# Kernel tuning notes

Measured on AMD Instinct MI355X. Metric: run time of the kernel, lower is better.

Reference implementation:

```python
import jax, jax.numpy as jnp
import numpy as np

B, G, L, S = 4096, 16000, 64, 20000  # batch spots, genes, labels, total spots
LOG_2PI = float(np.log(2.0 * np.pi))


def _log_nb_positive_altparam(x, r, o):
    # NB with total_count r > 0 and logits o (stereoscope parametrization)
    return (jax.lax.lgamma(x + r) - jax.lax.lgamma(r) - jax.lax.lgamma(x + 1.0)
            + x * jax.nn.log_sigmoid(o) + r * jax.nn.log_sigmoid(-o))


def setup_inputs() -> dict:
    key = jax.random.key(0)
    ks = jax.random.split(key, 8)
    x = jax.random.randint(ks[0], (B, G), 0, 100, dtype=jnp.int32)
    y = jax.random.randint(ks[1], (B, 1), 0, L, dtype=jnp.int32)
    ind_x = jax.random.randint(ks[2], (B, 1), 0, S, dtype=jnp.int32)
    W = jax.random.normal(ks[3], (G, L), dtype=jnp.float32)          # fixed dictionary
    px_o = 0.5 * jax.random.normal(ks[4], (G,), dtype=jnp.float32)   # fixed log-odds
    eta = jax.random.normal(ks[5], (G,), dtype=jnp.float32)
    V = jax.random.normal(ks[6], (L + 1, S), dtype=jnp.float32)
    beta = 0.1 * jax.random.normal(ks[7], (G,), dtype=jnp.float32)
    return {"x": x, "y": y, "ind_x": ind_x, "W": W, "px_o": px_o,
            "eta": eta, "V": V, "beta": beta}


def reference(x, y, ind_x, W, px_o, eta, V, beta):
    x_f = x.astype(jnp.float32)                      # [B, G]
    beta_sp = jax.nn.softplus(beta)                  # [G]
    w_sp = jax.nn.softplus(W)                        # [G, L]
    eps_sp = jax.nn.softplus(eta)                    # [G]
    # r_hat = [beta*W | eps]  -> [G, L+1]
    r_hat = jnp.concatenate([beta_sp[:, None] * w_sp, eps_sp[:, None]], axis=1)
    # column-gather from V (embedding lookup over spots), then softplus
    v_ind = jax.nn.softplus(V[:, ind_x[:, 0]])       # [L+1, B]
    # thin matmul, inner dim L+1; px_rate: [B, G]
    px_rate = jnp.einsum("gl,lb->bg", r_hat, v_ind)
    # NB reconstruction loss per spot
    reconst_loss = -jnp.sum(_log_nb_positive_altparam(x_f, px_rate, px_o[None, :]), axis=-1)  # [B]
    # -sum log N(eta; 0, 1)
    neg_log_likelihood_prior = jnp.sum(0.5 * LOG_2PI + 0.5 * eta * eta)
    return (reconst_loss, jnp.float32(0.0), neg_log_likelihood_prior)
```

## Files before the change

kernel.cpp:

```cpp
#include <hip/hip_runtime.h>
#include <hip/hip_bf16.h>
#include <math.h>

#define Gn 16000
#define Bn 4096
#define Ln 64
#define Sn 20000
#define NGT 250

typedef __attribute__((ext_vector_type(8))) short bf16x8;
typedef __attribute__((ext_vector_type(4))) float f32x4;


__device__ __forceinline__ float softplus_precise(float z) {
    return fmaxf(z, 0.0f) + log1pf(__expf(-fabsf(z)));
}

__device__ __forceinline__ float lgamma_pos8(float z) {
    float p = z * (z + 1.f) * (z + 2.f) * (z + 3.f)
                * (z + 4.f) * (z + 5.f) * (z + 6.f) * (z + 7.f);
    float w = z + 8.f;
    return (w - 0.5f) * __logf(w) - w + 0.9189385332046727f
           + __fdividef(1.0f, 12.0f * w) - __logf(p);
}

__device__ __forceinline__ unsigned short f2bf(float f) {
    union { float f; unsigned int u; } v; v.f = f;
    unsigned int r = v.u + 0x7fff + ((v.u >> 16) & 1);
    return (unsigned short)(r >> 16);
}


__global__ void prep_genes(const float* __restrict__ W,
                           const float* __restrict__ px_o,
                           const float* __restrict__ eta,
                           const float* __restrict__ beta,
                           unsigned short* __restrict__ rhB,
                           float* __restrict__ lsp1,
                           float* __restrict__ lsn,
                           float* __restrict__ eps,
                           float* __restrict__ out) {
    int idx = blockIdx.x * 256 + threadIdx.x;
    int g = idx >> 6;
    float bsp = softplus_precise(beta[g]);
    rhB[idx] = f2bf(bsp * softplus_precise(W[idx]));
    float s = 0.f;
    if (idx < Gn) {
        eps[idx] = softplus_precise(eta[idx]);
        float o = px_o[idx];
        lsp1[idx] = -softplus_precise(-o) - 1.0f;
        lsn[idx]  = -softplus_precise(o);
        float e = eta[idx];
        s = 0.9189385332046727f + 0.5f * e * e;
    }
    #pragma unroll
    for (int off = 32; off; off >>= 1) s += __shfl_xor(s, off, 64);
    __shared__ float red[4];
    if ((threadIdx.x & 63) == 0) red[threadIdx.x >> 6] = s;
    __syncthreads();
    if (threadIdx.x == 0) {
        float t = red[0] + red[1] + red[2] + red[3];
        if (t != 0.f) atomicAdd(&out[Bn + 1], t);
    }
}

__global__ void prep_spots(const float* __restrict__ V,
                           const int* __restrict__ ind_x,
                           unsigned short* __restrict__ vBg,
                           float* __restrict__ v64) {
    int idx = blockIdx.x * 256 + threadIdx.x;
    int b = idx >> 6, l = idx & 63;
    int s = ind_x[b];
    vBg[idx] = f2bf(softplus_precise(V[l * Sn + s]));
    if (idx < Bn) {
        int s2 = ind_x[idx];
        v64[idx] = softplus_precise(V[Ln * Sn + s2]);
    }
}


__global__ __launch_bounds__(256) void main_kernel(
    const int*            __restrict__ x,
    const unsigned short* __restrict__ rhB,
    const unsigned short* __restrict__ vBg,
    const float*          __restrict__ v64,
    const float*          __restrict__ lsp1g,
    const float*          __restrict__ lsng,
    const float*          __restrict__ epsg,
    float*                __restrict__ partial) {
    __shared__ __align__(16) unsigned short sA[64][72];
    __shared__ __align__(16) unsigned short sB[64][72];
    __shared__ float sv64[64];
    __shared__ float sLsp1[64], sLsn[64], sEps[64];
    __shared__ float lfact[100];
    __shared__ float pred[64];

    const int tid = threadIdx.x;
    const int b0 = blockIdx.x * 64;
    const int g0 = blockIdx.y * 64;

    {
        int row = tid >> 3;
        int c   = (tid & 7) * 8;
        *(uint4*)&sA[row][c]      = *(const uint4*)&vBg[(b0 + row) * 64 + c];
        *(uint4*)&sA[row + 32][c] = *(const uint4*)&vBg[(b0 + row + 32) * 64 + c];
        *(uint4*)&sB[row][c]      = *(const uint4*)&rhB[(g0 + row) * 64 + c];
        *(uint4*)&sB[row + 32][c] = *(const uint4*)&rhB[(g0 + row + 32) * 64 + c];
    }
    if (tid < 64) {
        sv64[tid]  = v64[b0 + tid];
        sLsp1[tid] = lsp1g[g0 + tid];
        sLsn[tid]  = lsng[g0 + tid];
        sEps[tid]  = epsg[g0 + tid];
    }
    if (tid < 100) lfact[tid] = lgamma_pos8((float)tid + 1.0f);

    const int wave = tid >> 6, lane = tid & 63;
    const int quad = lane >> 4, ln = lane & 15;
    const int mrow  = wave * 16 + ln;
    const int brow0 = b0 + wave * 16 + quad * 4;

    int xv[4][4];
    #pragma unroll
    for (int nb = 0; nb < 4; nb++) {
        int g = g0 + nb * 16 + ln;
        #pragma unroll
        for (int r = 0; r < 4; r++)
            xv[nb][r] = x[(size_t)(brow0 + r) * Gn + g];
    }

    f32x4 acc[4];
    #pragma unroll
    for (int nb = 0; nb < 4; nb++) acc[nb] = (f32x4){0.f, 0.f, 0.f, 0.f};

    __syncthreads();

    #pragma unroll
    for (int kb = 0; kb < 2; kb++) {
        bf16x8 af = *(const bf16x8*)&sA[mrow][kb * 32 + quad * 8];
        #pragma unroll
        for (int nb = 0; nb < 4; nb++) {
            bf16x8 bfr = *(const bf16x8*)&sB[nb * 16 + ln][kb * 32 + quad * 8];
            acc[nb] = __builtin_amdgcn_mfma_f32_16x16x32_bf16(af, bfr, acc[nb], 0, 0, 0);
        }
    }

    float vvr[4];
    #pragma unroll
    for (int r = 0; r < 4; r++) vvr[r] = sv64[wave * 16 + quad * 4 + r];

    float rowpart[4] = {0.f, 0.f, 0.f, 0.f};
    #pragma unroll
    for (int nb = 0; nb < 4; nb++) {
        const float lsp1v = sLsp1[nb * 16 + ln];
        const float lsnv  = sLsn[nb * 16 + ln];
        const float ev    = sEps[nb * 16 + ln];
        #pragma unroll
        for (int r = 0; r < 4; r++) {
            const float rr = fmaf(ev, vvr[r], acc[nb][r]);
            const int   xi = xv[nb][r];
            const float xf = (float)xi;
            const float s  = rr + xf;
            float t = fmaf(s - 0.5f, __logf(s), -lfact[xi]);
            t = fmaf(-(rr - 0.5f), __logf(rr), t);
            t = fmaf(xf, lsp1v, t);
            t = fmaf(rr, lsnv, t);
            rowpart[r] += t;
        }
    }

    #pragma unroll
    for (int r = 0; r < 4; r++) {
        float v = rowpart[r];
        v += __shfl_xor(v, 1, 64);
        v += __shfl_xor(v, 2, 64);
        v += __shfl_xor(v, 4, 64);
        v += __shfl_xor(v, 8, 64);
        if (ln == 0) pred[wave * 16 + quad * 4 + r] = v;
    }
    __syncthreads();
    if (tid < 64) partial[(size_t)blockIdx.y * Bn + b0 + tid] = pred[tid];
}

__global__ __launch_bounds__(256) void reduce_kernel(const float* __restrict__ partial,
                                                     float* __restrict__ out) {
    int b = blockIdx.x * 256 + threadIdx.x;
    float s0 = 0.f, s1 = 0.f, s2 = 0.f, s3 = 0.f, s4 = 0.f;
    for (int i = 0; i < NGT; i += 5) {
        s0 += partial[(size_t)(i + 0) * Bn + b];
        s1 += partial[(size_t)(i + 1) * Bn + b];
        s2 += partial[(size_t)(i + 2) * Bn + b];
        s3 += partial[(size_t)(i + 3) * Bn + b];
        s4 += partial[(size_t)(i + 4) * Bn + b];
    }
    out[b] = -(s0 + s1 + s2 + s3 + s4);
}


extern "C" void kernel_launch(void* const* d_in, const int* in_sizes, int n_in,
                              void* d_out, int out_size, void* d_ws, size_t ws_size,
                              hipStream_t stream) {
    const int*   x     = (const int*)d_in[0];
    const int*   ind_x = (const int*)d_in[2];
    const float* W     = (const float*)d_in[3];
    const float* px_o  = (const float*)d_in[4];
    const float* eta   = (const float*)d_in[5];
    const float* V     = (const float*)d_in[6];
    const float* beta  = (const float*)d_in[7];
    float* out = (float*)d_out;

    char* wsb = (char*)d_ws;
    unsigned short* rhB  = (unsigned short*)(wsb);
    unsigned short* vBg  = (unsigned short*)(wsb + 2048000);
    float*          v64  = (float*)(wsb + 2572288);
    float*          lsp1 = (float*)(wsb + 2588672);
    float*          lsn  = (float*)(wsb + 2652672);
    float*          eps  = (float*)(wsb + 2716672);
    float*          part = (float*)(wsb + 2780672);

    hipMemsetAsync(d_out, 0, (Bn + 2) * sizeof(float), stream);

    prep_genes<<<(Gn * 64) / 256, 256, 0, stream>>>(W, px_o, eta, beta, rhB, lsp1, lsn, eps, out);
    prep_spots<<<(Bn * 64) / 256, 256, 0, stream>>>(V, ind_x, vBg, v64);

    dim3 grid(Bn / 64, Gn / 64);
    main_kernel<<<grid, 256, 0, stream>>>(x, rhB, vBg, v64, lsp1, lsn, eps, part);

    reduce_kernel<<<Bn / 256, 256, 0, stream>>>(part, out);
}
```

Before: 413.0 us.

## Fuse prep kernels, drop memset and atomic, reorder main grid gene-major

Merges the gene and spot preprocessing kernels into one launch that branches on block index. The memset and the atomic prior accumulation are replaced by per-block partial sums that the reduce kernel combines; the reduce kernel also writes the zero output directly. The main kernel's grid is swapped so adjacent blocks cover adjacent gene tiles of the same spot rows, which changes the DRAM and cache access order for the large x matrix. The goal is lower launch overhead and better locality, at the cost of a slightly larger reduce kernel.

```diff
diff --git a/kernel.cpp b/kernel.cpp
--- a/kernel.cpp
+++ b/kernel.cpp
@@ -7,6 +7,8 @@
 #define Ln 64
 #define Sn 20000
 #define NGT 250
+#define GENE_BLOCKS 4000
+#define SPOT_BLOCKS 1024
 
 typedef __attribute__((ext_vector_type(8))) short bf16x8;
 typedef __attribute__((ext_vector_type(4))) float f32x4;
@@ -31,50 +33,52 @@
 }
 
 
-__global__ void prep_genes(const float* __restrict__ W,
+__global__ void prep_fused(const float* __restrict__ W,
                            const float* __restrict__ px_o,
                            const float* __restrict__ eta,
                            const float* __restrict__ beta,
+                           const float* __restrict__ V,
+                           const int*   __restrict__ ind_x,
                            unsigned short* __restrict__ rhB,
                            float* __restrict__ lsp1,
                            float* __restrict__ lsn,
                            float* __restrict__ eps,
-                           float* __restrict__ out) {
-    int idx = blockIdx.x * 256 + threadIdx.x;
-    int g = idx >> 6;
-    float bsp = softplus_precise(beta[g]);
-    rhB[idx] = f2bf(bsp * softplus_precise(W[idx]));
-    float s = 0.f;
-    if (idx < Gn) {
-        eps[idx] = softplus_precise(eta[idx]);
-        float o = px_o[idx];
-        lsp1[idx] = -softplus_precise(-o) - 1.0f;
-        lsn[idx]  = -softplus_precise(o);
-        float e = eta[idx];
-        s = 0.9189385332046727f + 0.5f * e * e;
-    }
-    #pragma unroll
-    for (int off = 32; off; off >>= 1) s += __shfl_xor(s, off, 64);
-    __shared__ float red[4];
-    if ((threadIdx.x & 63) == 0) red[threadIdx.x >> 6] = s;
-    __syncthreads();
-    if (threadIdx.x == 0) {
-        float t = red[0] + red[1] + red[2] + red[3];
-        if (t != 0.f) atomicAdd(&out[Bn + 1], t);
-    }
-}
-
-__global__ void prep_spots(const float* __restrict__ V,
-                           const int* __restrict__ ind_x,
                            unsigned short* __restrict__ vBg,
-                           float* __restrict__ v64) {
-    int idx = blockIdx.x * 256 + threadIdx.x;
-    int b = idx >> 6, l = idx & 63;
-    int s = ind_x[b];
-    vBg[idx] = f2bf(softplus_precise(V[l * Sn + s]));
-    if (idx < Bn) {
-        int s2 = ind_x[idx];
-        v64[idx] = softplus_precise(V[Ln * Sn + s2]);
+                           float* __restrict__ v64,
+                           float* __restrict__ prior_part) {
+    const int bid = blockIdx.x;
+    const int tid = threadIdx.x;
+    if (bid < GENE_BLOCKS) {
+        int idx = bid * 256 + tid;
+        int g = idx >> 6;
+        float bsp = softplus_precise(beta[g]);
+        rhB[idx] = f2bf(bsp * softplus_precise(W[idx]));
+        float s = 0.f;
+        if (idx < Gn) {
+            eps[idx] = softplus_precise(eta[idx]);
+            float o = px_o[idx];
+            lsp1[idx] = -softplus_precise(-o) - 1.0f;
+            lsn[idx]  = -softplus_precise(o);
+            float e = eta[idx];
+            s = 0.9189385332046727f + 0.5f * e * e;
+        }
+        if (bid < 64) {
+            #pragma unroll
+            for (int off = 32; off; off >>= 1) s += __shfl_xor(s, off, 64);
+            __shared__ float red[4];
+            if ((tid & 63) == 0) red[tid >> 6] = s;
+            __syncthreads();
+            if (tid == 0) prior_part[bid] = red[0] + red[1] + red[2] + red[3];
+        }
+    } else {
+        int idx = (bid - GENE_BLOCKS) * 256 + tid;
+        int b = idx >> 6, l = idx & 63;
+        int s = ind_x[b];
+        vBg[idx] = f2bf(softplus_precise(V[l * Sn + s]));
+        if (idx < Bn) {
+            int s2 = ind_x[idx];
+            v64[idx] = softplus_precise(V[Ln * Sn + s2]);
+        }
     }
 }
 
@@ -96,8 +100,8 @@
     __shared__ float pred[64];
 
     const int tid = threadIdx.x;
-    const int b0 = blockIdx.x * 64;
-    const int g0 = blockIdx.y * 64;
+    const int g0 = blockIdx.x * 64;
+    const int b0 = blockIdx.y * 64;
 
     {
         int row = tid >> 3;
@@ -179,10 +183,11 @@
         if (ln == 0) pred[wave * 16 + quad * 4 + r] = v;
     }
     __syncthreads();
-    if (tid < 64) partial[(size_t)blockIdx.y * Bn + b0 + tid] = pred[tid];
+    if (tid < 64) partial[(size_t)blockIdx.x * Bn + b0 + tid] = pred[tid];
 }
 
 __global__ __launch_bounds__(256) void reduce_kernel(const float* __restrict__ partial,
+                                                     const float* __restrict__ prior_part,
                                                      float* __restrict__ out) {
     int b = blockIdx.x * 256 + threadIdx.x;
     float s0 = 0.f, s1 = 0.f, s2 = 0.f, s3 = 0.f, s4 = 0.f;
@@ -194,6 +199,19 @@
         s4 += partial[(size_t)(i + 4) * Bn + b];
     }
     out[b] = -(s0 + s1 + s2 + s3 + s4);
+
+    if (blockIdx.x == 0) {
+        int tid = threadIdx.x;
+        if (tid < 64) {
+            float s = prior_part[tid];
+            #pragma unroll
+            for (int off = 32; off; off >>= 1) s += __shfl_xor(s, off, 64);
+            if (tid == 0) {
+                out[Bn]     = 0.0f;
+                out[Bn + 1] = s;
+            }
+        }
+    }
 }
 
 
@@ -210,21 +228,20 @@
     float* out = (float*)d_out;
 
     char* wsb = (char*)d_ws;
-    unsigned short* rhB  = (unsigned short*)(wsb);
-    unsigned short* vBg  = (unsigned short*)(wsb + 2048000);
-    float*          v64  = (float*)(wsb + 2572288);
-    float*          lsp1 = (float*)(wsb + 2588672);
-    float*          lsn  = (float*)(wsb + 2652672);
-    float*          eps  = (float*)(wsb + 2716672);
-    float*          part = (float*)(wsb + 2780672);
-
-    hipMemsetAsync(d_out, 0, (Bn + 2) * sizeof(float), stream);
-
-    prep_genes<<<(Gn * 64) / 256, 256, 0, stream>>>(W, px_o, eta, beta, rhB, lsp1, lsn, eps, out);
-    prep_spots<<<(Bn * 64) / 256, 256, 0, stream>>>(V, ind_x, vBg, v64);
-
-    dim3 grid(Bn / 64, Gn / 64);
+    unsigned short* rhB   = (unsigned short*)(wsb);
+    unsigned short* vBg   = (unsigned short*)(wsb + 2048000);
+    float*          v64   = (float*)(wsb + 2572288);
+    float*          lsp1  = (float*)(wsb + 2588672);
+    float*          lsn   = (float*)(wsb + 2652672);
+    float*          eps   = (float*)(wsb + 2716672);
+    float*          part  = (float*)(wsb + 2780672);
+    float*          prio  = (float*)(wsb + 6876672);
+
+    prep_fused<<<GENE_BLOCKS + SPOT_BLOCKS, 256, 0, stream>>>(
+        W, px_o, eta, beta, V, ind_x, rhB, lsp1, lsn, eps, vBg, v64, prio);
+
+    dim3 grid(Gn / 64, Bn / 64);
     main_kernel<<<grid, 256, 0, stream>>>(x, rhB, vBg, v64, lsp1, lsn, eps, part);
 
-    reduce_kernel<<<Bn / 256, 256, 0, stream>>>(part, out);
-}
+    reduce_kernel<<<Bn / 256, 256, 0, stream>>>(part, prio, out);
+}
```

After: 391.2 us. 1.06x faster.
